# Performance work log

Hardware: AMD Instinct MI355X
Metric: run time of the kernel (lower is better)

## Reference

```python
import jax, jax.numpy as jnp
import numpy as np

N, E, F_IN, C = 50000, 800000, 128, 300
NEG_SLOPE = 0.2  # PyG GATv2Conv default negative_slope


def setup_inputs() -> dict:
    key = jax.random.key(0)
    ks = jax.random.split(key, 10)
    x = jax.random.normal(ks[0], (N, F_IN), dtype=jnp.float32)
    edge_index = jax.random.randint(ks[1], (2, E), 0, N, dtype=jnp.int64)
    s_in = np.float32(1.0 / np.sqrt(F_IN))
    s_c = np.float32(1.0 / np.sqrt(C))
    Wl = jax.random.normal(ks[2], (F_IN, C), dtype=jnp.float32) * s_in
    bl = jnp.zeros((C,), jnp.float32)
    Wr = jax.random.normal(ks[3], (F_IN, C), dtype=jnp.float32) * s_in
    br = jnp.zeros((C,), jnp.float32)
    att = jax.random.normal(ks[4], (C,), dtype=jnp.float32) * s_c
    bias = jnp.zeros((C,), jnp.float32)
    lw = jax.random.normal(ks[5], (C, 1), dtype=jnp.float32) * s_c
    lb = jnp.zeros((1,), jnp.float32)
    return {"x": x, "edge_index": edge_index, "Wl": Wl, "bl": bl,
            "Wr": Wr, "br": br, "att": att, "bias": bias, "lw": lw, "lb": lb}


def reference(x, edge_index, Wl, bl, Wr, br, att, bias, lw, lb):
    n = x.shape[0]
    # GATv2: separate source/target linear transforms
    xl = x @ Wl + bl  # [N, C] (source / message features)
    xr = x @ Wr + br  # [N, C] (target features)
    # add self loops (PyG default add_self_loops=True)
    loops = jnp.arange(n, dtype=edge_index.dtype)
    src = jnp.concatenate([edge_index[0], loops])  # [E+N]
    dst = jnp.concatenate([edge_index[1], loops])  # [E+N]
    # GATv2 attention logit: a^T LeakyReLU(xl_j + xr_i)
    e = jax.nn.leaky_relu(xl[src] + xr[dst], NEG_SLOPE) @ att  # [E+N]
    # segment softmax over incoming edges of each target node
    m = jax.ops.segment_max(e, dst, num_segments=n)
    ex = jnp.exp(e - m[dst])
    denom = jax.ops.segment_sum(ex, dst, num_segments=n)
    alpha = ex / denom[dst]  # [E+N]
    # weighted scatter-aggregation of source messages + conv bias
    out = jax.ops.segment_sum(xl[src] * alpha[:, None], dst, num_segments=n) + bias
    h = jax.nn.relu(out)          # torch.relu
    # F.dropout in eval mode is identity (reference is inference math)
    return jax.nn.sigmoid(h @ lw + lb)  # [N, 1]
```

## Files before the change

### kernel.cpp

```cpp
#include <hip/hip_runtime.h>
#include <hip/hip_fp16.h>

#define F_IN 128
#define C_DIM 300
#define NEG_SLOPE 0.2f
#define NCT  40
#define CH   8
#define NPB  256

typedef _Float16 half8 __attribute__((ext_vector_type(8)));
typedef _Float16 half4 __attribute__((ext_vector_type(4)));
typedef _Float16 h2    __attribute__((ext_vector_type(2)));
typedef float    f32x4 __attribute__((ext_vector_type(4)));
typedef float    f32x2 __attribute__((ext_vector_type(2)));

__device__ inline h2 as_h2(unsigned u) { union { unsigned u; h2 h; } c; c.u = u; return c.h; }
__device__ inline unsigned as_u(h2 h)  { union { unsigned u; h2 h; } c; c.h = h; return c.u; }
__device__ inline f32x2 upv(unsigned u) {
    h2 h = as_h2(u);
    f32x2 r; r.x = (float)h.x; r.y = (float)h.y; return r;
}

#if __has_builtin(__builtin_amdgcn_fdot2)
__device__ inline float fdot2w(h2 a, h2 b, float c) {
    return __builtin_amdgcn_fdot2(a, b, c, false);
}
#else
__device__ inline float fdot2w(h2 a, h2 b, float c) {
    return fmaf((float)a.y, (float)b.y, fmaf((float)a.x, (float)b.x, c));
}
#endif

__global__ __launch_bounds__(256) void convert_w(
    const float* __restrict__ Wl, const float* __restrict__ Wr,
    _Float16* __restrict__ Bp)
{
    int idx = blockIdx.x * 256 + threadIdx.x;
    if (idx >= 640 * F_IN) return;
    int nn = idx % 640;
    int k  = idx / 640;
    float v = 0.f;
    if (nn < 300)                   v = Wl[k * C_DIM + nn];
    else if (nn >= 304 && nn < 604) v = Wr[k * C_DIM + (nn - 304)];
    int ct = nn >> 4, n16 = nn & 15;
    int kr = k & 31,  ks  = k >> 5;
    int lane = ((kr >> 3) << 4) | n16;
    int j = k & 7;
    Bp[((((ct * 4 + ks) * 64) + lane) << 3) | j] = (_Float16)v;
}

__global__ __launch_bounds__(256) void gemm_xlxr(
    const float* __restrict__ x, const _Float16* __restrict__ Bp,
    const float* __restrict__ bl, const float* __restrict__ br,
    _Float16* __restrict__ xlh, _Float16* __restrict__ xrh, int n)
{
    __shared__ __align__(16) _Float16 xs[64][136];
    const int rb0 = blockIdx.x * 64;
    const int t   = threadIdx.x;

    #pragma unroll
    for (int i = 0; i < 8; ++i) {
        int flat = (i * 256 + t) * 4;
        int r = flat >> 7;
        int k = flat & 127;
        int gr = rb0 + r;
        if (gr >= n) gr = n - 1;
        float4 v = *reinterpret_cast<const float4*>(x + (size_t)gr * F_IN + k);
        half4 h = { (_Float16)v.x, (_Float16)v.y, (_Float16)v.z, (_Float16)v.w };
        *reinterpret_cast<half4*>(&xs[r][k]) = h;
    }
    __syncthreads();

    const int w    = t >> 6;
    const int lane = t & 63;
    const int m    = lane & 15;
    const int quad = lane >> 4;

    half8 a[4];
    #pragma unroll
    for (int ks = 0; ks < 4; ++ks)
        a[ks] = *reinterpret_cast<const half8*>(&xs[w * 16 + m][ks * 32 + quad * 8]);

    const int rbase = rb0 + w * 16 + quad * 4;

    #pragma unroll 4
    for (int ct = 0; ct < NCT; ++ct) {
        f32x4 acc = {0.f, 0.f, 0.f, 0.f};
        #pragma unroll
        for (int ks = 0; ks < 4; ++ks) {
            half8 b = *reinterpret_cast<const half8*>(
                Bp + (((size_t)(ct * 4 + ks) * 64 + lane) << 3));
            acc = __builtin_amdgcn_mfma_f32_16x16x32_f16(a[ks], b, acc, 0, 0, 0);
        }
        int col = ct * 16 + m;
        int isL = (col < 300);
        int isR = (col >= 304 && col < 604);
        if (isL | isR) {
            float bv = isL ? bl[col] : br[col - 304];
            _Float16* tab = isL ? (xlh + col) : (xrh + (col - 304));
            #pragma unroll
            for (int reg = 0; reg < 4; ++reg) {
                int row = rbase + reg;
                if (row < n)
                    tab[(size_t)row * C_DIM] = (_Float16)(acc[reg] + bv);
            }
        }
    }
}

__global__ __launch_bounds__(256) void bucket_count(
    const int* __restrict__ dst, unsigned* __restrict__ bcnt, int nE, int chunk)
{
    __shared__ unsigned cnt[256];
    const int b = blockIdx.x, t = threadIdx.x;
    cnt[t] = 0;
    __syncthreads();
    const int lo = b * chunk;
    const int hi = min(nE, lo + chunk);
    for (int i = lo + t; i < hi; i += 256)
        atomicAdd(&cnt[dst[i] >> 8], 1u);
    __syncthreads();
    bcnt[t * NPB + b] = cnt[t];
}

__global__ __launch_bounds__(256) void scan_part(
    const unsigned* __restrict__ counts, unsigned* __restrict__ bsum, int n)
{
    __shared__ unsigned s[256];
    const int t = threadIdx.x;
    const int base = blockIdx.x * 1024 + t * 4;
    unsigned v = 0;
    #pragma unroll
    for (int i = 0; i < 4; ++i) {
        int idx = base + i;
        if (idx < n) v += counts[idx];
    }
    s[t] = v;
    __syncthreads();
    for (int off = 128; off > 0; off >>= 1) {
        if (t < off) s[t] += s[t + off];
        __syncthreads();
    }
    if (t == 0) bsum[blockIdx.x] = s[0];
}

__global__ __launch_bounds__(64) void scan_mid(
    unsigned* __restrict__ bsum, unsigned* __restrict__ offs, int nblk, int n)
{
    const int lane = threadIdx.x;
    unsigned v = (lane < nblk) ? bsum[lane] : 0u;
    unsigned inc = v;
    #pragma unroll
    for (int off = 1; off < 64; off <<= 1) {
        unsigned u = __shfl_up(inc, off);
        if (lane >= off) inc += u;
    }
    if (lane < nblk) bsum[lane] = inc - v;
    if (lane == 63) offs[n] = inc;
}

__global__ __launch_bounds__(256) void scan_final(
    const unsigned* __restrict__ counts, const unsigned* __restrict__ bsum,
    unsigned* __restrict__ offs, unsigned* __restrict__ cursor, int n)
{
    __shared__ unsigned s[256];
    const int t = threadIdx.x;
    const int base = blockIdx.x * 1024 + t * 4;
    unsigned c[4];
    unsigned v = 0;
    #pragma unroll
    for (int i = 0; i < 4; ++i) {
        int idx = base + i;
        c[i] = (idx < n) ? counts[idx] : 0u;
        v += c[i];
    }
    s[t] = v;
    __syncthreads();
    for (int off = 1; off < 256; off <<= 1) {
        unsigned u = (t >= off) ? s[t - off] : 0u;
        __syncthreads();
        if (t >= off) s[t] += u;
        __syncthreads();
    }
    unsigned run = bsum[blockIdx.x] + s[t] - v;
    #pragma unroll
    for (int i = 0; i < 4; ++i) {
        int idx = base + i;
        if (idx < n) {
            offs[idx] = run;
            cursor[idx] = run;
            run += c[i];
        }
    }
}

__global__ __launch_bounds__(256) void partition_edges(
    const int* __restrict__ src, const int* __restrict__ dst,
    const unsigned* __restrict__ boff,
    int* __restrict__ ebuf_src, int* __restrict__ ebuf_dst, int nE, int chunk)
{
    __shared__ unsigned cur[256];
    const int b = blockIdx.x, t = threadIdx.x;
    cur[t] = boff[t * NPB + b];
    __syncthreads();
    const int lo = b * chunk;
    const int hi = min(nE, lo + chunk);
    for (int i = lo + t; i < hi; i += 256) {
        int d  = dst[i];
        int sv = src[i];
        unsigned p = atomicAdd(&cur[d >> 8], 1u);
        ebuf_src[p] = sv;
        ebuf_dst[p] = d;
    }
}

__global__ __launch_bounds__(256) void bucket_csr(
    const int* __restrict__ ebuf_src, const int* __restrict__ ebuf_dst,
    const unsigned* __restrict__ boff, unsigned* __restrict__ offs,
    int* __restrict__ csr_src, int n, int nE, int nb)
{
    __shared__ unsigned cnt[256];
    __shared__ unsigned s[256];
    __shared__ unsigned cur[256];
    const int bk = blockIdx.x;
    const int t  = threadIdx.x;
    const unsigned bstart = boff[(unsigned)bk * NPB];
    const unsigned bend   = boff[(unsigned)(bk + 1) * NPB];
    cnt[t] = 0;
    __syncthreads();
    for (unsigned i = bstart + t; i < bend; i += 256)
        atomicAdd(&cnt[ebuf_dst[i] & 255], 1u);
    __syncthreads();
    unsigned v = cnt[t];
    s[t] = v;
    __syncthreads();
    for (int off = 1; off < 256; off <<= 1) {
        unsigned u = (t >= off) ? s[t - off] : 0u;
        __syncthreads();
        if (t >= off) s[t] += u;
        __syncthreads();
    }
    const unsigned excl = s[t] - v;
    const int node = (bk << 8) + t;
    if (node <= n) offs[node] = bstart + excl;
    if (t == 0 && bk == nb - 1 && (n & 255) == 0) offs[n] = (unsigned)nE;
    cur[t] = bstart + excl;
    __syncthreads();
    for (unsigned i = bstart + t; i < bend; i += 256) {
        int d = ebuf_dst[i];
        unsigned p = atomicAdd(&cur[d & 255], 1u);
        csr_src[p] = ebuf_src[i];
    }
}

__global__ __launch_bounds__(256) void gat_gather(
    const int* __restrict__ csr_src, const unsigned* __restrict__ offs,
    const _Float16* __restrict__ xlh, const _Float16* __restrict__ xrh,
    const float* __restrict__ att, const float* __restrict__ bias,
    const float* __restrict__ lw, const float* __restrict__ lb,
    float* __restrict__ y, int n)
{
    __shared__ __align__(16) float lds[4 * 560];
    float* part = lds + (threadIdx.x >> 6) * 560;

    const int wid  = (blockIdx.x * blockDim.x + threadIdx.x) >> 6;
    const int lane = threadIdx.x & 63;
    if (wid >= n) return;

    const int l2   = 2 * lane;
    const bool has2 = (lane < 22);
    const int t8   = lane & 7;
    const int o    = lane >> 3;
    const int byteoff = lane * 4;

    const _Float16* xrrow = xrh + (size_t)wid * C_DIM;
    h2 xr0 = *(const h2*)(xrrow + l2);
    h2 xr1 = *(const h2*)(xrrow + 128 + l2);
    h2 xr2 = {(_Float16)0, (_Float16)0};
    if (has2) xr2 = *(const h2*)(xrrow + 256 + l2);

    h2 a06[3], a04[3];
    #pragma unroll
    for (int k = 0; k < 3; ++k) {
        int c = 128 * k + l2;
        float ax = (c < C_DIM) ? att[c] : 0.f;
        float ay = (c + 1 < C_DIM) ? att[c + 1] : 0.f;
        a06[k].x = (_Float16)(0.6f * ax); a06[k].y = (_Float16)(0.6f * ay);
        a04[k].x = (_Float16)(0.4f * ax); a04[k].y = (_Float16)(0.4f * ay);
    }

    f32x2 acc2[3] = {{0.f, 0.f}, {0.f, 0.f}, {0.f, 0.f}};
    float den_l = 0.f;

    const unsigned start = offs[wid];
    const int totalE = (int)(offs[wid + 1] - start) + 1;
    const char* basep = (const char*)xlh;

    for (int base = 0; base < totalE; base += CH) {
        int idv = wid;
        {
            int k = base + lane;
            if (lane < CH && k > 0 && k < totalE) idv = csr_src[start + k - 1];
        }
        int rowb = idv * (C_DIM * 2);
        int ro[CH];
        #pragma unroll
        for (int tt = 0; tt < CH; ++tt) ro[tt] = __shfl(rowb, tt);

        unsigned pk0[CH], pk1[CH], pk2[CH];
        #pragma unroll
        for (int tt = 0; tt < CH; ++tt) {
            const char* p = basep + ro[tt] + byteoff;
            pk0[tt] = *(const unsigned*)(p);
            pk1[tt] = *(const unsigned*)(p + 256);
            pk2[tt] = 0u;
        }
        if (has2) {
            #pragma unroll
            for (int tt = 0; tt < CH; ++tt)
                pk2[tt] = *(const unsigned*)(basep + ro[tt] + byteoff + 512);
        }

        #pragma unroll
        for (int tt = 0; tt < CH; ++tt) {
            h2 z0 = as_h2(pk0[tt]) + xr0;
            h2 z1 = as_h2(pk1[tt]) + xr1;
            h2 z2 = as_h2(pk2[tt]) + xr2;
            float p = fdot2w(z0, a06[0], 0.f);
            p = fdot2w(as_h2(as_u(z0) & 0x7FFF7FFFu), a04[0], p);
            p = fdot2w(z1, a06[1], p);
            p = fdot2w(as_h2(as_u(z1) & 0x7FFF7FFFu), a04[1], p);
            p = fdot2w(z2, a06[2], p);
            p = fdot2w(as_h2(as_u(z2) & 0x7FFF7FFFu), a04[2], p);
            part[tt * 68 + lane] = p;
        }

        float wgt;
        {
            const int oo = (o + t8) & 7;
            const float* rp = part + t8 * 68 + oo * 8;
            float4 s0 = *(const float4*)(rp + 0);
            float4 s1 = *(const float4*)(rp + 4);
            float e = ((s0.x + s0.y) + (s0.z + s0.w)) + ((s1.x + s1.y) + (s1.z + s1.w));
            e += __shfl_xor(e, 8);
            e += __shfl_xor(e, 16);
            e += __shfl_xor(e, 32);
            bool valid = (base + t8) < totalE;
            wgt = valid ? __expf(fminf(e, 60.f)) : 0.f;
        }

        den_l += wgt;

        _Float16 wh = (_Float16)wgt;
        h2 wpair = {wh, wh};
        unsigned wbits = as_u(wpair);
        h2 hacc0 = {(_Float16)0, (_Float16)0};
        h2 hacc1 = {(_Float16)0, (_Float16)0};
        h2 hacc2 = {(_Float16)0, (_Float16)0};
        #pragma unroll
        for (int tt = 0; tt < CH; ++tt) {
            h2 wt2 = as_h2(__shfl(wbits, tt));
            hacc0 += wt2 * as_h2(pk0[tt]);
            hacc1 += wt2 * as_h2(pk1[tt]);
            hacc2 += wt2 * as_h2(pk2[tt]);
        }
        acc2[0] += upv(as_u(hacc0));
        acc2[1] += upv(as_u(hacc1));
        acc2[2] += upv(as_u(hacc2));
    }

    float den = den_l;
    den += __shfl_xor(den, 1);
    den += __shfl_xor(den, 2);
    den += __shfl_xor(den, 4);

    const float invd = 1.f / den;
    float dot = 0.f;
    #pragma unroll
    for (int k = 0; k < 3; ++k) {
        #pragma unroll
        for (int j = 0; j < 2; ++j) {
            int c = 128 * k + l2 + j;
            float b = (c < C_DIM) ? bias[c] : 0.f;
            float l = (c < C_DIM) ? lw[c] : 0.f;
            float a = (j == 0) ? acc2[k].x : acc2[k].y;
            float h = fmaf(a, invd, b);
            h = h > 0.f ? h : 0.f;
            dot = fmaf(h, l, dot);
        }
    }
    #pragma unroll
    for (int off = 32; off; off >>= 1) dot += __shfl_xor(dot, off);
    if (lane == 0) y[wid] = 1.f / (1.f + __expf(-(dot + lb[0])));
}

extern "C" void kernel_launch(void* const* d_in, const int* in_sizes, int n_in,
                              void* d_out, int out_size, void* d_ws, size_t ws_size,
                              hipStream_t stream)
{
    const float* x    = (const float*)d_in[0];
    const int*   ei   = (const int*)d_in[1];
    const float* Wl   = (const float*)d_in[2];
    const float* bl   = (const float*)d_in[3];
    const float* Wr   = (const float*)d_in[4];
    const float* br   = (const float*)d_in[5];
    const float* att  = (const float*)d_in[6];
    const float* bias = (const float*)d_in[7];
    const float* lw   = (const float*)d_in[8];
    const float* lb   = (const float*)d_in[9];
    float* y = (float*)d_out;

    const int n  = in_sizes[0] / F_IN;
    const int nE = in_sizes[1] / 2;
    const int* src_arr = ei;
    const int* dst_arr = ei + nE;

    const int NB    = (n + 255) >> 8;
    const int chunk = (nE + NPB - 1) / NPB;
    const int M     = 256 * NPB;
    const int nblkM = (M + 1023) / 1024;

    _Float16* xlh      = (_Float16*)d_ws;
    _Float16* xrh      = xlh + (size_t)n * C_DIM;
    _Float16* Bp       = xrh + (size_t)n * C_DIM;
    unsigned* bcnt     = (unsigned*)(Bp + NCT * 4 * 64 * 8);
    unsigned* boff     = bcnt + M;
    unsigned* offs     = boff + (M + 1);
    unsigned* bsum     = offs + (n + 1);
    int*      csr_src  = (int*)(bsum + 64);
    int*      ebuf_src = csr_src + nE;
    int*      ebuf_dst = ebuf_src + nE;

    convert_w<<<(640 * F_IN + 255) / 256, 256, 0, stream>>>(Wl, Wr, Bp);

    bucket_count<<<NPB, 256, 0, stream>>>(dst_arr, bcnt, nE, chunk);
    scan_part<<<nblkM, 256, 0, stream>>>(bcnt, bsum, M);
    scan_mid<<<1, 64, 0, stream>>>(bsum, boff, nblkM, M);
    scan_final<<<nblkM, 256, 0, stream>>>(bcnt, bsum, boff, (unsigned*)ebuf_dst, M);
    partition_edges<<<NPB, 256, 0, stream>>>(src_arr, dst_arr, boff, ebuf_src, ebuf_dst, nE, chunk);
    bucket_csr<<<NB, 256, 0, stream>>>(ebuf_src, ebuf_dst, boff, offs, csr_src, n, nE, NB);

    gemm_xlxr<<<(n + 63) / 64, 256, 0, stream>>>(x, Bp, bl, br, xlh, xrh, n);

    gat_gather<<<(n + 3) / 4, 256, 0, stream>>>(csr_src, offs, xlh, xrh, att, bias, lw, lb, y, n);
}
```

Baseline: 259.4 us.

## Fuse scan stages, pack edge buffer, and prefetch next CSR chunk in gather

Merges the middle scan kernel into the final scan so each block recomputes the block-sum prefix with a wavefront scan. Drops an unused cursor write. Packs source id and the low byte of the destination into one 32-bit word, halving edge-buffer traffic in partition and bucket kernels. In the gather kernel, the next chunk's neighbor indices are loaded while the current feature loads are in flight. Packing assumes node ids fit in 16 bits.

```diff
diff --git a/kernel.cpp b/kernel.cpp
--- a/kernel.cpp
+++ b/kernel.cpp
@@ -144,27 +144,24 @@
     if (t == 0) bsum[blockIdx.x] = s[0];
 }
 
-__global__ __launch_bounds__(64) void scan_mid(
-    unsigned* __restrict__ bsum, unsigned* __restrict__ offs, int nblk, int n)
-{
-    const int lane = threadIdx.x;
-    unsigned v = (lane < nblk) ? bsum[lane] : 0u;
-    unsigned inc = v;
-    #pragma unroll
-    for (int off = 1; off < 64; off <<= 1) {
-        unsigned u = __shfl_up(inc, off);
-        if (lane >= off) inc += u;
-    }
-    if (lane < nblk) bsum[lane] = inc - v;
-    if (lane == 63) offs[n] = inc;
-}
-
 __global__ __launch_bounds__(256) void scan_final(
     const unsigned* __restrict__ counts, const unsigned* __restrict__ bsum,
-    unsigned* __restrict__ offs, unsigned* __restrict__ cursor, int n)
+    unsigned* __restrict__ offs, int n, int nblk)
 {
     __shared__ unsigned s[256];
+    __shared__ unsigned sbase;
     const int t = threadIdx.x;
+    if (t < 64) {
+        unsigned v64 = (t < nblk) ? bsum[t] : 0u;
+        unsigned inc = v64;
+        #pragma unroll
+        for (int off = 1; off < 64; off <<= 1) {
+            unsigned u = __shfl_up(inc, off);
+            if (t >= off) inc += u;
+        }
+        if (t == (int)blockIdx.x) sbase = inc - v64;
+        if (blockIdx.x == gridDim.x - 1 && t == 63) offs[n] = inc;
+    }
     const int base = blockIdx.x * 1024 + t * 4;
     unsigned c[4];
     unsigned v = 0;
@@ -182,13 +179,12 @@
         if (t >= off) s[t] += u;
         __syncthreads();
     }
-    unsigned run = bsum[blockIdx.x] + s[t] - v;
+    unsigned run = sbase + s[t] - v;
     #pragma unroll
     for (int i = 0; i < 4; ++i) {
         int idx = base + i;
         if (idx < n) {
             offs[idx] = run;
-            cursor[idx] = run;
             run += c[i];
         }
     }
@@ -197,7 +193,7 @@
 __global__ __launch_bounds__(256) void partition_edges(
     const int* __restrict__ src, const int* __restrict__ dst,
     const unsigned* __restrict__ boff,
-    int* __restrict__ ebuf_src, int* __restrict__ ebuf_dst, int nE, int chunk)
+    unsigned* __restrict__ ebuf, int nE, int chunk)
 {
     __shared__ unsigned cur[256];
     const int b = blockIdx.x, t = threadIdx.x;
@@ -209,15 +205,13 @@
         int d  = dst[i];
         int sv = src[i];
         unsigned p = atomicAdd(&cur[d >> 8], 1u);
-        ebuf_src[p] = sv;
-        ebuf_dst[p] = d;
+        ebuf[p] = (unsigned)sv | ((unsigned)(d & 255) << 16);
     }
 }
 
 __global__ __launch_bounds__(256) void bucket_csr(
-    const int* __restrict__ ebuf_src, const int* __restrict__ ebuf_dst,
-    const unsigned* __restrict__ boff, unsigned* __restrict__ offs,
-    int* __restrict__ csr_src, int n, int nE, int nb)
+    const unsigned* __restrict__ ebuf, const unsigned* __restrict__ boff,
+    unsigned* __restrict__ offs, int* __restrict__ csr_src, int n, int nE, int nb)
 {
     __shared__ unsigned cnt[256];
     __shared__ unsigned s[256];
@@ -229,7 +223,7 @@
     cnt[t] = 0;
     __syncthreads();
     for (unsigned i = bstart + t; i < bend; i += 256)
-        atomicAdd(&cnt[ebuf_dst[i] & 255], 1u);
+        atomicAdd(&cnt[(ebuf[i] >> 16) & 255], 1u);
     __syncthreads();
     unsigned v = cnt[t];
     s[t] = v;
@@ -247,9 +241,9 @@
     cur[t] = bstart + excl;
     __syncthreads();
     for (unsigned i = bstart + t; i < bend; i += 256) {
-        int d = ebuf_dst[i];
-        unsigned p = atomicAdd(&cur[d & 255], 1u);
-        csr_src[p] = ebuf_src[i];
+        unsigned e = ebuf[i];
+        unsigned p = atomicAdd(&cur[(e >> 16) & 255], 1u);
+        csr_src[p] = (int)(e & 0xFFFFu);
     }
 }
 
@@ -296,12 +290,13 @@
     const int totalE = (int)(offs[wid + 1] - start) + 1;
     const char* basep = (const char*)xlh;
 
+    int idv = wid;
+    {
+        int k = lane;
+        if (lane < CH && k > 0 && k < totalE) idv = csr_src[start + k - 1];
+    }
+
     for (int base = 0; base < totalE; base += CH) {
-        int idv = wid;
-        {
-            int k = base + lane;
-            if (lane < CH && k > 0 && k < totalE) idv = csr_src[start + k - 1];
-        }
         int rowb = idv * (C_DIM * 2);
         int ro[CH];
         #pragma unroll
@@ -319,6 +314,12 @@
             #pragma unroll
             for (int tt = 0; tt < CH; ++tt)
                 pk2[tt] = *(const unsigned*)(basep + ro[tt] + byteoff + 512);
+        }
+
+        idv = wid;
+        {
+            int k = base + CH + lane;
+            if (lane < CH && k > 0 && k < totalE) idv = csr_src[start + k - 1];
         }
 
         #pragma unroll
@@ -428,17 +429,15 @@
     unsigned* offs     = boff + (M + 1);
     unsigned* bsum     = offs + (n + 1);
     int*      csr_src  = (int*)(bsum + 64);
-    int*      ebuf_src = csr_src + nE;
-    int*      ebuf_dst = ebuf_src + nE;
+    unsigned* ebuf     = (unsigned*)(csr_src + nE);
 
     convert_w<<<(640 * F_IN + 255) / 256, 256, 0, stream>>>(Wl, Wr, Bp);
 
     bucket_count<<<NPB, 256, 0, stream>>>(dst_arr, bcnt, nE, chunk);
     scan_part<<<nblkM, 256, 0, stream>>>(bcnt, bsum, M);
-    scan_mid<<<1, 64, 0, stream>>>(bsum, boff, nblkM, M);
-    scan_final<<<nblkM, 256, 0, stream>>>(bcnt, bsum, boff, (unsigned*)ebuf_dst, M);
-    partition_edges<<<NPB, 256, 0, stream>>>(src_arr, dst_arr, boff, ebuf_src, ebuf_dst, nE, chunk);
-    bucket_csr<<<NB, 256, 0, stream>>>(ebuf_src, ebuf_dst, boff, offs, csr_src, n, nE, NB);
+    scan_final<<<nblkM, 256, 0, stream>>>(bcnt, bsum, boff, M, nblkM);
+    partition_edges<<<NPB, 256, 0, stream>>>(src_arr, dst_arr, boff, ebuf, nE, chunk);
+    bucket_csr<<<NB, 256, 0, stream>>>(ebuf, boff, offs, csr_src, n, nE, NB);
 
     gemm_xlxr<<<(n + 63) / 64, 256, 0, stream>>>(x, Bp, bl, br, xlh, xrh, n);
 
```

After: 243.8 us. 6.0% less time.
